# Performance work log

Hardware: AMD Instinct MI355X
Metric: run time of the kernel (lower is better)

Reference implementation:

```python
import jax, jax.numpy as jnp
import numpy as np
import math

N, S, T, D = 4, 2048, 2048, 1024

def setup_inputs() -> dict:
    key = jax.random.key(0)
    ks = jax.random.split(key, 6)
    scale = 1.0 / math.sqrt(D)
    return {
        "query": jax.random.normal(ks[0], (N, S, D), dtype=jnp.float32),
        "key": jax.random.normal(ks[1], (N, T, D), dtype=jnp.float32),
        "value": jax.random.normal(ks[2], (N, T, D), dtype=jnp.float32),
        # causal mask: 1 = attend, 0 = masked out (masked_fill where mask == 0)
        "attn_mask": jnp.tril(jnp.ones((S, T), dtype=jnp.int32)),
        "Wq": jax.random.normal(ks[3], (D, D), dtype=jnp.float32) * scale,
        "Wk": jax.random.normal(ks[4], (D, D), dtype=jnp.float32) * scale,
        "Wv": jax.random.normal(ks[5], (D, D), dtype=jnp.float32) * scale,
    }

def reference(query, key, value, attn_mask, Wq, Wk, Wv):
    # nn.Linear(bias=False): y = x @ W.T
    q = jnp.einsum('nsd,ed->nse', query, Wq)
    k = jnp.einsum('ntd,ed->nte', key, Wk)
    v = jnp.einsum('ntd,ed->nte', value, Wv)
    # scaled dot-product scores [N, S, T]
    dot = jnp.einsum('nse,nte->nst', q, k) / jnp.sqrt(jnp.asarray(D, q.dtype))
    dot = jnp.where(attn_mask == 0, -jnp.inf, dot)
    scores = jax.nn.softmax(dot, axis=-1)
    # dropout is identity in eval mode
    y = jnp.einsum('nst,nte->nse', scores, v)
    return y
```

## Files before the change

kernel.cpp:

```cpp
#include <hip/hip_runtime.h>
#include <math.h>

using u16 = unsigned short;
typedef __attribute__((ext_vector_type(8))) __bf16 bf16x8;
typedef __attribute__((ext_vector_type(4))) float f32x4;
typedef __attribute__((ext_vector_type(4))) float f4v;
typedef __attribute__((ext_vector_type(8))) u16 u16x8;

__device__ __forceinline__ u16 f2bf(float f) {
  unsigned u = __float_as_uint(f);
  u += 0x7fffu + ((u >> 16) & 1u);
  return (u16)(u >> 16);
}
__device__ __forceinline__ float bf2f(u16 b) {
  unsigned u = ((unsigned)b) << 16;
  return __uint_as_float(u);
}

__device__ __forceinline__ void gload16(const void* g, void* l) {
  __builtin_amdgcn_global_load_lds(
      (const __attribute__((address_space(1))) unsigned int*)g,
      (__attribute__((address_space(3))) unsigned int*)l, 16, 0, 0);
}

__device__ __forceinline__ f32x4 MF(bf16x8 a, bf16x8 b, f32x4 c) {
  return __builtin_amdgcn_mfma_f32_16x16x32_bf16(a, b, c, 0, 0, 0);
}

__global__ __launch_bounds__(256) void cast3_f32_bf16(
    const float* __restrict__ p0, const float* __restrict__ p1,
    const float* __restrict__ p2, u16* __restrict__ out, size_t ostride) {
  int z = blockIdx.z;
  const float* in = (z == 0) ? p0 : (z == 1) ? p1 : p2;
  size_t i = ((size_t)blockIdx.x * 256 + threadIdx.x) * 8;
  f4v a = *reinterpret_cast<const f4v*>(in + i);
  f4v b = *reinterpret_cast<const f4v*>(in + i + 4);
  u16x8 r;
  r[0] = f2bf(a[0]); r[1] = f2bf(a[1]); r[2] = f2bf(a[2]); r[3] = f2bf(a[3]);
  r[4] = f2bf(b[0]); r[5] = f2bf(b[1]); r[6] = f2bf(b[2]); r[7] = f2bf(b[3]);
  *reinterpret_cast<u16x8*>(out + z * ostride + i) = r;
}

__global__ __launch_bounds__(256) void wprep(
    const float* __restrict__ Wk, const float* __restrict__ Wq,
    const float* __restrict__ Wv, u16* __restrict__ wkT,
    u16* __restrict__ wqT, u16* __restrict__ wv_bf) {
  int z = blockIdx.z;
  if (z < 2) {
    __shared__ float t[64][65];
    const float* I = z ? Wq : Wk;
    u16* O = z ? wqT : wkT;
    int c0 = blockIdx.x * 64, r0 = blockIdx.y * 64;
    int tx = threadIdx.x & 63, ty = threadIdx.x >> 6;
    #pragma unroll
    for (int i = 0; i < 64; i += 4)
      t[ty + i][tx] = I[(size_t)(r0 + ty + i) * 1024 + c0 + tx];
    __syncthreads();
    #pragma unroll
    for (int i = 0; i < 64; i += 4)
      O[(size_t)(c0 + ty + i) * 1024 + r0 + tx] = f2bf(t[tx][ty + i]);
  } else {
    int b = blockIdx.y * 16 + blockIdx.x;
    size_t i = (size_t)b * 4096 + threadIdx.x * 16;
    #pragma unroll
    for (int h = 0; h < 2; ++h) {
      f4v a = *reinterpret_cast<const f4v*>(Wv + i + h * 8);
      f4v c = *reinterpret_cast<const f4v*>(Wv + i + h * 8 + 4);
      u16x8 r;
      r[0] = f2bf(a[0]); r[1] = f2bf(a[1]); r[2] = f2bf(a[2]); r[3] = f2bf(a[3]);
      r[4] = f2bf(c[0]); r[5] = f2bf(c[1]); r[6] = f2bf(c[2]); r[7] = f2bf(c[3]);
      *reinterpret_cast<u16x8*>(wv_bf + i + h * 8) = r;
    }
  }
}

template<typename OutT, int MODE>
__global__ __launch_bounds__(512) void gemm_bt8(
    const u16* __restrict__ A, const u16* __restrict__ B, OutT* __restrict__ C,
    int K, int lda, int ldb, int ldc,
    size_t sA, size_t sB, size_t sC, float alpha,
    OutT* __restrict__ C1) {
  int bn, bm, bz = 0;
  int kEnd = K;
  bool whichV = false;
  const u16 *Ag, *Bg;
  OutT* Cg;
  if (MODE == 0) {
    bm = blockIdx.x >> 3;
    bn = blockIdx.x & 7;
    Ag = A + (size_t)bm * 128 * lda;
    Bg = B + (size_t)bn * 128 * ldb;
    Cg = C;
  } else if (MODE == 1) {
    int h = blockIdx.x;
    int l = (h & 7) * 68 + (h >> 3);
    bz = l / 136;
    int t = l % 136;
    bm = (int)((sqrtf(8.f * (float)t + 1.f) - 1.f) * 0.5f);
    while ((bm + 1) * (bm + 2) / 2 <= t) ++bm;
    while (bm * (bm + 1) / 2 > t) --bm;
    bn = t - bm * (bm + 1) / 2;
    Ag = A + sA * bz + (size_t)bm * 128 * lda;
    Bg = B + sB * bz + (size_t)bn * 128 * ldb;
    Cg = C + sC * bz;
  } else if (MODE == 2) {
    int l = blockIdx.x;
    bm = 15 - (l >> 5);
    int rest = l & 31;
    bz = rest >> 3;
    bn = rest & 7;
    kEnd = (K < (bm + 1) * 128) ? K : (bm + 1) * 128;
    Ag = A + sA * bz + (size_t)bm * 128 * lda;
    Bg = B + sB * bz + (size_t)bn * 128 * ldb;
    Cg = C + sC * bz;
  } else {
    int h = blockIdx.x;
    int l = (h & 7) * 128 + (h >> 3);
    bn = l & 7;
    int bm128 = l >> 3;
    whichV = (bm128 >> 6) != 0;
    bm = bm128 & 63;
    if (whichV) {
      Ag = B + sB + (size_t)bn * 128 * ldb;
      Bg = A + (size_t)bm128 * 128 * lda;
    } else {
      Ag = A + (size_t)bm128 * 128 * lda;
      Bg = B + (size_t)bn * 128 * ldb;
    }
    Cg = C;
  }

  __shared__ __align__(16) u16 As[2][128 * 32];
  __shared__ __align__(16) u16 Bs[2][128 * 32];

  const int tid = threadIdx.x;
  const int lane = tid & 63, wv = tid >> 6;
  const int wr = wv >> 2, wc = wv & 3;
  const int fr = lane & 15, kq = (lane >> 4) * 8;
  const int g4 = (lane >> 4) * 4;

  const int e0 = wv * 512 + lane * 8;
  const int r0 = e0 >> 5, c0 = e0 & 31;
  const u16* a0 = Ag + (size_t)r0 * lda + c0;
  const u16* b0 = Bg + (size_t)r0 * ldb + c0;

  f32x4 acc[4][2] = {};
  const int nt = kEnd / 32;

  gload16(a0, &As[0][wv * 512]);
  gload16(b0, &Bs[0][wv * 512]);
  __syncthreads();

  for (int t = 0; t < nt; ++t) {
    const int cur = t & 1;
    if (t + 1 < nt) {
      const int k0 = (t + 1) * 32;
      gload16(a0 + k0, &As[cur ^ 1][wv * 512]);
      gload16(b0 + k0, &Bs[cur ^ 1][wv * 512]);
    }
    bf16x8 af[4], bfv[2];
    #pragma unroll
    for (int m = 0; m < 4; ++m)
      af[m] = *reinterpret_cast<const bf16x8*>(&As[cur][(wr * 64 + m * 16 + fr) * 32 + kq]);
    #pragma unroll
    for (int n = 0; n < 2; ++n)
      bfv[n] = *reinterpret_cast<const bf16x8*>(&Bs[cur][(wc * 32 + n * 16 + fr) * 32 + kq]);
    #pragma unroll
    for (int m = 0; m < 4; ++m)
      #pragma unroll
      for (int n = 0; n < 2; ++n)
        acc[m][n] = MF(af[m], bfv[n], acc[m][n]);
    __syncthreads();
  }

  if constexpr (MODE == 3) {
    if (whichV) {
      const int eb = bn * 128 + wr * 64 + g4;
      const int tb = (bm & 15) * 128 + wc * 32 + fr;
      const size_t zoff = (size_t)(bm >> 4) * (1024 * 2048);
      #pragma unroll
      for (int m = 0; m < 4; ++m)
        #pragma unroll
        for (int n = 0; n < 2; ++n)
          #pragma unroll
          for (int j = 0; j < 4; ++j)
            C1[zoff + (size_t)(eb + m * 16 + j) * 2048 + (tb + n * 16)] =
                f2bf(acc[m][n][j]);
      return;
    }
  }

  const int row0 = bm * 128 + wr * 64 + g4;
  const int col0 = bn * 128 + wc * 32 + fr;
  #pragma unroll
  for (int m = 0; m < 4; ++m)
    #pragma unroll
    for (int n = 0; n < 2; ++n) {
      #pragma unroll
      for (int j = 0; j < 4; ++j) {
        float val = acc[m][n][j] * alpha;
        size_t idx = (size_t)(row0 + m * 16 + j) * ldc + (col0 + n * 16);
        if constexpr (sizeof(OutT) == 2) Cg[idx] = f2bf(val);
        else Cg[idx] = val;
      }
    }
}

__global__ __launch_bounds__(256) void softmax_causal(u16* __restrict__ sc) {
  int r = blockIdx.x;
  int s = r & 2047;
  u16* row = sc + (size_t)r * 2048;
  int tid = threadIdx.x;
  int t0 = tid * 8;
  u16x8 raw = {0, 0, 0, 0, 0, 0, 0, 0};
  if (t0 <= s) raw = *reinterpret_cast<const u16x8*>(row + t0);
  float v[8];
  float mx = -1e30f;
  #pragma unroll
  for (int j = 0; j < 8; ++j) {
    v[j] = ((t0 + j) <= s) ? bf2f(raw[j]) : -1e30f;
    mx = fmaxf(mx, v[j]);
  }
  #pragma unroll
  for (int o = 32; o; o >>= 1) mx = fmaxf(mx, __shfl_xor(mx, o, 64));
  __shared__ float red[8];
  if ((tid & 63) == 0) red[tid >> 6] = mx;
  __syncthreads();
  mx = fmaxf(fmaxf(red[0], red[1]), fmaxf(red[2], red[3]));
  float p[8];
  float sum = 0.f;
  #pragma unroll
  for (int j = 0; j < 8; ++j) {
    p[j] = ((t0 + j) <= s) ? __expf(v[j] - mx) : 0.f;
    sum += p[j];
  }
  #pragma unroll
  for (int o = 32; o; o >>= 1) sum += __shfl_xor(sum, o, 64);
  if ((tid & 63) == 0) red[4 + (tid >> 6)] = sum;
  __syncthreads();
  sum = red[4] + red[5] + red[6] + red[7];
  float inv = 1.0f / sum;
  u16x8 o8;
  #pragma unroll
  for (int j = 0; j < 8; ++j) o8[j] = f2bf(p[j] * inv);
  if (t0 <= (s | 127))
    *reinterpret_cast<u16x8*>(row + t0) = o8;
}

extern "C" void kernel_launch(void* const* d_in, const int* in_sizes, int n_in,
                              void* d_out, int out_size, void* d_ws, size_t ws_size,
                              hipStream_t stream) {
  const float* q  = (const float*)d_in[0];
  const float* k  = (const float*)d_in[1];
  const float* v  = (const float*)d_in[2];
  const float* Wq = (const float*)d_in[4];
  const float* Wk = (const float*)d_in[5];
  const float* Wv = (const float*)d_in[6];
  float* out = (float*)d_out;
  char* ws = (char*)d_ws;

  const size_t MB = 1024ull * 1024ull;
  u16* sc   = (u16*)ws;
  u16* qb   = (u16*)ws;
  u16* xk   = (u16*)(ws + 32 * MB);
  u16* wsl  = (u16*)(ws + 48 * MB);
  u16* wkT  = (u16*)(ws + 52 * MB);
  u16* wqT  = (u16*)(ws + 54 * MB);
  u16* Vt   = (u16*)(ws + 56 * MB);
  u16* Yq   = (u16*)(ws + 72 * MB);
  (void)in_sizes; (void)n_in; (void)out_size; (void)ws_size;

  wprep<<<dim3(16, 16, 3), 256, 0, stream>>>(Wk, Wq, Wv, wkT, wqT,
                                             wsl + 1048576);

  gemm_bt8<u16, 0><<<64, 512, 0, stream>>>(
      wkT, wqT, wsl, 1024, 1024, 1024, 1024, 0, 0, 0, 1.0f, nullptr);

  cast3_f32_bf16<<<dim3(4096, 1, 3), 256, 0, stream>>>(q, v, k, qb, 8ull * MB);

  gemm_bt8<u16, 3><<<1024, 512, 0, stream>>>(
      qb, wsl, Yq, 1024, 1024, 1024, 1024,
      0, 1048576, 0, 1.0f, Vt);

  gemm_bt8<u16, 1><<<544, 512, 0, stream>>>(
      Yq, xk, sc, 1024, 1024, 1024, 2048,
      (size_t)2048 * 1024, (size_t)2048 * 1024, (size_t)2048 * 2048, 0.03125f,
      nullptr);

  softmax_causal<<<8192, 256, 0, stream>>>(sc);

  gemm_bt8<float, 2><<<512, 512, 0, stream>>>(
      sc, Vt, out, 2048, 2048, 2048, 1024,
      (size_t)2048 * 2048, (size_t)1024 * 2048, (size_t)2048 * 1024, 1.0f,
      nullptr);
}
```

Baseline: 171.6 us.

## Add 256x256-tile pipelined projection GEMM and merge prep kernels

Replaces the 128x128-tile projection GEMM (MODE 3) with a dedicated 256x256-tile kernel that uses swizzled LDS layouts, a 128 KB double buffer, staged global-to-LDS prefetch with explicit waitcnt and barriers, and s_setprio around the MFMA bursts. It also merges the weight preparation and input cast kernels into one launch. The goal is more data reuse per tile and better overlap of loads with MFMA work, plus one fewer launch. The cost is only 256 blocks at occupancy 1, which risks under-filling the CUs, and the hand-placed waitcnt/barrier schedule is fragile.

```diff
diff --git a/kernel.cpp b/kernel.cpp
--- a/kernel.cpp
+++ b/kernel.cpp
@@ -27,30 +27,36 @@
   return __builtin_amdgcn_mfma_f32_16x16x32_bf16(a, b, c, 0, 0, 0);
 }
 
-__global__ __launch_bounds__(256) void cast3_f32_bf16(
-    const float* __restrict__ p0, const float* __restrict__ p1,
-    const float* __restrict__ p2, u16* __restrict__ out, size_t ostride) {
-  int z = blockIdx.z;
-  const float* in = (z == 0) ? p0 : (z == 1) ? p1 : p2;
-  size_t i = ((size_t)blockIdx.x * 256 + threadIdx.x) * 8;
-  f4v a = *reinterpret_cast<const f4v*>(in + i);
-  f4v b = *reinterpret_cast<const f4v*>(in + i + 4);
-  u16x8 r;
-  r[0] = f2bf(a[0]); r[1] = f2bf(a[1]); r[2] = f2bf(a[2]); r[3] = f2bf(a[3]);
-  r[4] = f2bf(b[0]); r[5] = f2bf(b[1]); r[6] = f2bf(b[2]); r[7] = f2bf(b[3]);
-  *reinterpret_cast<u16x8*>(out + z * ostride + i) = r;
-}
-
-__global__ __launch_bounds__(256) void wprep(
-    const float* __restrict__ Wk, const float* __restrict__ Wq,
-    const float* __restrict__ Wv, u16* __restrict__ wkT,
-    u16* __restrict__ wqT, u16* __restrict__ wv_bf) {
-  int z = blockIdx.z;
-  if (z < 2) {
-    __shared__ float t[64][65];
+#define BARX() __builtin_amdgcn_s_barrier()
+#define LGKM0() asm volatile("s_waitcnt lgkmcnt(0)" ::: "memory")
+#define VMW4() asm volatile("s_waitcnt vmcnt(4)" ::: "memory")
+#define VMW0() asm volatile("s_waitcnt vmcnt(0)" ::: "memory")
+
+__global__ __launch_bounds__(256) void prep(
+    const float* __restrict__ q, const float* __restrict__ v,
+    const float* __restrict__ k, const float* __restrict__ Wk,
+    const float* __restrict__ Wq, const float* __restrict__ Wv,
+    u16* __restrict__ qb, u16* __restrict__ wkT, u16* __restrict__ wqT,
+    u16* __restrict__ wv_bf) {
+  __shared__ float t[64][65];
+  int b = blockIdx.x;
+  if (b < 12288) {
+    int z = b >> 12;
+    int bb = b & 4095;
+    const float* in = (z == 0) ? q : (z == 1) ? v : k;
+    size_t i = ((size_t)bb * 256 + threadIdx.x) * 8;
+    f4v a = *reinterpret_cast<const f4v*>(in + i);
+    f4v c = *reinterpret_cast<const f4v*>(in + i + 4);
+    u16x8 r;
+    r[0] = f2bf(a[0]); r[1] = f2bf(a[1]); r[2] = f2bf(a[2]); r[3] = f2bf(a[3]);
+    r[4] = f2bf(c[0]); r[5] = f2bf(c[1]); r[6] = f2bf(c[2]); r[7] = f2bf(c[3]);
+    *reinterpret_cast<u16x8*>(qb + (size_t)z * 8388608 + i) = r;
+  } else if (b < 12800) {
+    int c = b - 12288;
+    int z = c >> 8, idx = c & 255;
     const float* I = z ? Wq : Wk;
     u16* O = z ? wqT : wkT;
-    int c0 = blockIdx.x * 64, r0 = blockIdx.y * 64;
+    int c0 = (idx & 15) * 64, r0 = (idx >> 4) * 64;
     int tx = threadIdx.x & 63, ty = threadIdx.x >> 6;
     #pragma unroll
     for (int i = 0; i < 64; i += 4)
@@ -60,8 +66,8 @@
     for (int i = 0; i < 64; i += 4)
       O[(size_t)(c0 + ty + i) * 1024 + r0 + tx] = f2bf(t[tx][ty + i]);
   } else {
-    int b = blockIdx.y * 16 + blockIdx.x;
-    size_t i = (size_t)b * 4096 + threadIdx.x * 16;
+    int bb = b - 12800;
+    size_t i = (size_t)bb * 4096 + threadIdx.x * 16;
     #pragma unroll
     for (int h = 0; h < 2; ++h) {
       f4v a = *reinterpret_cast<const f4v*>(Wv + i + h * 8);
@@ -74,23 +80,196 @@
   }
 }
 
+__global__ __launch_bounds__(512, 1) void proj256(
+    const u16* __restrict__ Xq, const u16* __restrict__ Xv,
+    const u16* __restrict__ Mt, const u16* __restrict__ Wv,
+    u16* __restrict__ Yq, u16* __restrict__ Vt) {
+  int h = blockIdx.x;
+  int l = (h & 7) * 32 + (h >> 3);
+  const bool wV = l >= 128;
+  int li = l & 127;
+  int bm, bn;
+  const u16 *Ag, *Bg;
+  if (!wV) {
+    bm = li >> 2; bn = li & 3;
+    Ag = Xq + (size_t)bm * 256 * 1024;
+    Bg = Mt + (size_t)bn * 256 * 1024;
+  } else {
+    bm = li & 3; bn = li >> 2;
+    Ag = Wv + (size_t)bm * 256 * 1024;
+    Bg = Xv + (size_t)bn * 256 * 1024;
+  }
+
+  __shared__ __align__(16) char sm[131072];
+
+  const int tid = threadIdx.x;
+  const int lane = tid & 63, wv = tid >> 6;
+  const int wr = wv >> 2, wc = wv & 3;
+  const int fr = lane & 15, hi = lane >> 4, fr7 = lane & 7;
+  const int l3 = lane >> 3;
+  const int colsw = ((lane & 7) ^ l3) * 8;
+  const int lnx16 = lane * 16;
+
+  const u16 *pA[2][2], *pB[2][2];
+  int ldsA[2][2], ldsB[2][2];
+  #pragma unroll
+  for (int hh = 0; hh < 2; ++hh)
+    #pragma unroll
+    for (int j = 0; j < 2; ++j) {
+      int row = hh * 128 + wv * 8 + j * 64 + l3;
+      pA[hh][j] = Ag + (size_t)row * 1024 + colsw;
+      pB[hh][j] = Bg + (size_t)row * 1024 + colsw;
+      ldsA[hh][j] = hh * 16384 + (wv + j * 8) * 1024 + lnx16;
+      ldsB[hh][j] = 32768 + ldsA[hh][j];
+    }
+
+  const int aBase = wr * 16384 + fr * 128;
+  const int bBase = 32768 + (wc >> 1) * 16384 + ((wc & 1) * 64 + fr) * 128;
+  const int sl0 = (hi ^ fr7) << 4;
+  const int sl1 = ((4 + hi) ^ fr7) << 4;
+
+#define RDA(buf, m, kk) (*(const bf16x8*)((buf) + aBase + (m) * 2048 + ((kk) ? sl1 : sl0)))
+#define RDB(buf, n, kk) (*(const bf16x8*)((buf) + bBase + (n) * 2048 + ((kk) ? sl1 : sl0)))
+
+  f32x4 acc[8][4] = {};
+  const int nt = 16;
+
+  {
+    char* b0 = sm;
+    gload16(pA[0][0], b0 + ldsA[0][0]); gload16(pA[0][1], b0 + ldsA[0][1]);
+    gload16(pA[1][0], b0 + ldsA[1][0]); gload16(pA[1][1], b0 + ldsA[1][1]);
+    gload16(pB[0][0], b0 + ldsB[0][0]); gload16(pB[0][1], b0 + ldsB[0][1]);
+    gload16(pB[1][0], b0 + ldsB[1][0]); gload16(pB[1][1], b0 + ldsB[1][1]);
+    char* b1 = sm + 65536;
+    gload16(pB[0][0] + 64, b1 + ldsB[0][0]); gload16(pB[0][1] + 64, b1 + ldsB[0][1]);
+    gload16(pB[1][0] + 64, b1 + ldsB[1][0]); gload16(pB[1][1] + 64, b1 + ldsB[1][1]);
+  }
+  VMW4();
+  BARX();
+
+  for (int t = 0; t < nt; ++t) {
+    const int cur = t & 1;
+    const char* buf = sm + cur * 65536;
+    char* nbuf = sm + (cur ^ 1) * 65536;
+    char* cbuf = sm + cur * 65536;
+    const bool st1 = (t + 1 < nt), st2 = (t + 2 < nt);
+    bf16x8 bf0[4], bf1[4];
+    bf16x8 a00, a01, a10, a11;
+
+    a00 = RDA(buf, 0, 0); a01 = RDA(buf, 0, 1);
+    a10 = RDA(buf, 1, 0); a11 = RDA(buf, 1, 1);
+    #pragma unroll
+    for (int n = 0; n < 4; ++n) { bf0[n] = RDB(buf, n, 0); bf1[n] = RDB(buf, n, 1); }
+    if (st1) {
+      gload16(pA[0][0] + (t + 1) * 64, nbuf + ldsA[0][0]);
+      gload16(pA[0][1] + (t + 1) * 64, nbuf + ldsA[0][1]);
+    }
+    BARX(); LGKM0();
+    __builtin_amdgcn_s_setprio(1);
+    #pragma unroll
+    for (int n = 0; n < 4; ++n) {
+      acc[0][n] = MF(a00, bf0[n], acc[0][n]);
+      acc[0][n] = MF(a01, bf1[n], acc[0][n]);
+      acc[1][n] = MF(a10, bf0[n], acc[1][n]);
+      acc[1][n] = MF(a11, bf1[n], acc[1][n]);
+    }
+    __builtin_amdgcn_s_setprio(0);
+    BARX();
+
+    a00 = RDA(buf, 2, 0); a01 = RDA(buf, 2, 1);
+    a10 = RDA(buf, 3, 0); a11 = RDA(buf, 3, 1);
+    if (st1) {
+      gload16(pA[1][0] + (t + 1) * 64, nbuf + ldsA[1][0]);
+      gload16(pA[1][1] + (t + 1) * 64, nbuf + ldsA[1][1]);
+    }
+    if (st2) {
+      gload16(pB[0][0] + (t + 2) * 64, cbuf + ldsB[0][0]);
+      gload16(pB[0][1] + (t + 2) * 64, cbuf + ldsB[0][1]);
+    }
+    BARX(); LGKM0();
+    __builtin_amdgcn_s_setprio(1);
+    #pragma unroll
+    for (int n = 0; n < 4; ++n) {
+      acc[2][n] = MF(a00, bf0[n], acc[2][n]);
+      acc[2][n] = MF(a01, bf1[n], acc[2][n]);
+      acc[3][n] = MF(a10, bf0[n], acc[3][n]);
+      acc[3][n] = MF(a11, bf1[n], acc[3][n]);
+    }
+    __builtin_amdgcn_s_setprio(0);
+    BARX();
+
+    a00 = RDA(buf, 4, 0); a01 = RDA(buf, 4, 1);
+    a10 = RDA(buf, 5, 0); a11 = RDA(buf, 5, 1);
+    if (st2) {
+      gload16(pB[1][0] + (t + 2) * 64, cbuf + ldsB[1][0]);
+      gload16(pB[1][1] + (t + 2) * 64, cbuf + ldsB[1][1]);
+    }
+    BARX(); LGKM0();
+    __builtin_amdgcn_s_setprio(1);
+    #pragma unroll
+    for (int n = 0; n < 4; ++n) {
+      acc[4][n] = MF(a00, bf0[n], acc[4][n]);
+      acc[4][n] = MF(a01, bf1[n], acc[4][n]);
+      acc[5][n] = MF(a10, bf0[n], acc[5][n]);
+      acc[5][n] = MF(a11, bf1[n], acc[5][n]);
+    }
+    __builtin_amdgcn_s_setprio(0);
+    BARX();
+
+    a00 = RDA(buf, 6, 0); a01 = RDA(buf, 6, 1);
+    a10 = RDA(buf, 7, 0); a11 = RDA(buf, 7, 1);
+    if (st2) { VMW4(); } else if (st1) { VMW0(); }
+    BARX(); LGKM0();
+    __builtin_amdgcn_s_setprio(1);
+    #pragma unroll
+    for (int n = 0; n < 4; ++n) {
+      acc[6][n] = MF(a00, bf0[n], acc[6][n]);
+      acc[6][n] = MF(a01, bf1[n], acc[6][n]);
+      acc[7][n] = MF(a10, bf0[n], acc[7][n]);
+      acc[7][n] = MF(a11, bf1[n], acc[7][n]);
+    }
+    __builtin_amdgcn_s_setprio(0);
+    BARX();
+  }
+
+  if (!wV) {
+    const int row0 = bm * 256 + wr * 128 + hi * 4;
+    const int col0 = bn * 256 + wc * 64 + fr;
+    #pragma unroll
+    for (int m = 0; m < 8; ++m)
+      #pragma unroll
+      for (int n = 0; n < 4; ++n)
+        #pragma unroll
+        for (int j = 0; j < 4; ++j)
+          Yq[(size_t)(row0 + m * 16 + j) * 1024 + (col0 + n * 16)] =
+              f2bf(acc[m][n][j]);
+  } else {
+    const int e0 = bm * 256 + wr * 128 + hi * 4;
+    const int t0 = (bn & 7) * 256 + wc * 64 + fr;
+    const size_t zoff = (size_t)(bn >> 3) * (1024 * 2048);
+    #pragma unroll
+    for (int m = 0; m < 8; ++m)
+      #pragma unroll
+      for (int n = 0; n < 4; ++n)
+        #pragma unroll
+        for (int j = 0; j < 4; ++j)
+          Vt[zoff + (size_t)(e0 + m * 16 + j) * 2048 + (t0 + n * 16)] =
+              f2bf(acc[m][n][j]);
+  }
+#undef RDA
+#undef RDB
+}
+
 template<typename OutT, int MODE>
 __global__ __launch_bounds__(512) void gemm_bt8(
     const u16* __restrict__ A, const u16* __restrict__ B, OutT* __restrict__ C,
     int K, int lda, int ldb, int ldc,
-    size_t sA, size_t sB, size_t sC, float alpha,
-    OutT* __restrict__ C1) {
+    size_t sA, size_t sB, size_t sC, float alpha) {
   int bn, bm, bz = 0;
   int kEnd = K;
-  bool whichV = false;
-  const u16 *Ag, *Bg;
-  OutT* Cg;
   if (MODE == 0) {
     bm = blockIdx.x >> 3;
     bn = blockIdx.x & 7;
-    Ag = A + (size_t)bm * 128 * lda;
-    Bg = B + (size_t)bn * 128 * ldb;
-    Cg = C;
   } else if (MODE == 1) {
     int h = blockIdx.x;
     int l = (h & 7) * 68 + (h >> 3);
@@ -100,35 +279,17 @@
     while ((bm + 1) * (bm + 2) / 2 <= t) ++bm;
     while (bm * (bm + 1) / 2 > t) --bm;
     bn = t - bm * (bm + 1) / 2;
-    Ag = A + sA * bz + (size_t)bm * 128 * lda;
-    Bg = B + sB * bz + (size_t)bn * 128 * ldb;
-    Cg = C + sC * bz;
-  } else if (MODE == 2) {
+  } else {
     int l = blockIdx.x;
     bm = 15 - (l >> 5);
     int rest = l & 31;
     bz = rest >> 3;
     bn = rest & 7;
     kEnd = (K < (bm + 1) * 128) ? K : (bm + 1) * 128;
-    Ag = A + sA * bz + (size_t)bm * 128 * lda;
-    Bg = B + sB * bz + (size_t)bn * 128 * ldb;
-    Cg = C + sC * bz;
-  } else {
-    int h = blockIdx.x;
-    int l = (h & 7) * 128 + (h >> 3);
-    bn = l & 7;
-    int bm128 = l >> 3;
-    whichV = (bm128 >> 6) != 0;
-    bm = bm128 & 63;
-    if (whichV) {
-      Ag = B + sB + (size_t)bn * 128 * ldb;
-      Bg = A + (size_t)bm128 * 128 * lda;
-    } else {
-      Ag = A + (size_t)bm128 * 128 * lda;
-      Bg = B + (size_t)bn * 128 * ldb;
-    }
-    Cg = C;
-  }
+  }
+  const u16* Ag = A + sA * bz + (size_t)bm * 128 * lda;
+  const u16* Bg = B + sB * bz + (size_t)bn * 128 * ldb;
+  OutT* Cg = C + sC * bz;
 
   __shared__ __align__(16) u16 As[2][128 * 32];
   __shared__ __align__(16) u16 Bs[2][128 * 32];
@@ -171,23 +332,6 @@
       for (int n = 0; n < 2; ++n)
         acc[m][n] = MF(af[m], bfv[n], acc[m][n]);
     __syncthreads();
-  }
-
-  if constexpr (MODE == 3) {
-    if (whichV) {
-      const int eb = bn * 128 + wr * 64 + g4;
-      const int tb = (bm & 15) * 128 + wc * 32 + fr;
-      const size_t zoff = (size_t)(bm >> 4) * (1024 * 2048);
-      #pragma unroll
-      for (int m = 0; m < 4; ++m)
-        #pragma unroll
-        for (int n = 0; n < 2; ++n)
-          #pragma unroll
-          for (int j = 0; j < 4; ++j)
-            C1[zoff + (size_t)(eb + m * 16 + j) * 2048 + (tb + n * 16)] =
-                f2bf(acc[m][n][j]);
-      return;
-    }
   }
 
   const int row0 = bm * 128 + wr * 64 + g4;
@@ -270,27 +414,22 @@
   u16* Yq   = (u16*)(ws + 72 * MB);
   (void)in_sizes; (void)n_in; (void)out_size; (void)ws_size;
 
-  wprep<<<dim3(16, 16, 3), 256, 0, stream>>>(Wk, Wq, Wv, wkT, wqT,
-                                             wsl + 1048576);
+  prep<<<13056, 256, 0, stream>>>(q, v, k, Wk, Wq, Wv, qb, wkT, wqT,
+                                  wsl + 1048576);
 
   gemm_bt8<u16, 0><<<64, 512, 0, stream>>>(
-      wkT, wqT, wsl, 1024, 1024, 1024, 1024, 0, 0, 0, 1.0f, nullptr);
-
-  cast3_f32_bf16<<<dim3(4096, 1, 3), 256, 0, stream>>>(q, v, k, qb, 8ull * MB);
-
-  gemm_bt8<u16, 3><<<1024, 512, 0, stream>>>(
-      qb, wsl, Yq, 1024, 1024, 1024, 1024,
-      0, 1048576, 0, 1.0f, Vt);
+      wkT, wqT, wsl, 1024, 1024, 1024, 1024, 0, 0, 0, 1.0f);
+
+  proj256<<<256, 512, 0, stream>>>(qb, qb + 8388608, wsl, wsl + 1048576,
+                                   Yq, Vt);
 
   gemm_bt8<u16, 1><<<544, 512, 0, stream>>>(
       Yq, xk, sc, 1024, 1024, 1024, 2048,
-      (size_t)2048 * 1024, (size_t)2048 * 1024, (size_t)2048 * 2048, 0.03125f,
-      nullptr);
+      (size_t)2048 * 1024, (size_t)2048 * 1024, (size_t)2048 * 2048, 0.03125f);
 
   softmax_causal<<<8192, 256, 0, stream>>>(sc);
 
   gemm_bt8<float, 2><<<512, 512, 0, stream>>>(
       sc, Vt, out, 2048, 2048, 2048, 1024,
-      (size_t)2048 * 2048, (size_t)1024 * 2048, (size_t)2048 * 1024, 1.0f,
-      nullptr);
-}
+      (size_t)2048 * 2048, (size_t)1024 * 2048, (size_t)2048 * 1024, 1.0f);
+}
```

After: 162.0 us. 1.06x faster.
